# Kernel tuning notes

Measured on AMD Instinct MI355X. Metric: run time of the kernel, lower is better.

## Reference

```python
import jax, jax.numpy as jnp
import numpy as np

N = 50000
E = 1600000
HID = 128
K = 2
EPS = 0.3


def setup_inputs() -> dict:
    key = jax.random.key(0)
    ks = jax.random.split(key, 8)
    x = jax.random.normal(ks[0], (N, 512), dtype=jnp.float32)
    edge_index = jax.random.randint(ks[1], (2, E), 0, N, dtype=jnp.int32)
    t1_w = jax.random.normal(ks[2], (HID, 512), dtype=jnp.float32) * (1.414 / np.sqrt(512))
    t1_b = jnp.zeros((HID,), dtype=jnp.float32)
    gate_w = jax.random.normal(ks[3], (K, 2 * HID), dtype=jnp.float32) * (1.414 / np.sqrt(2 * HID))
    gate_b = jnp.zeros((K,), dtype=jnp.float32)
    t2_w = jax.random.normal(ks[4], (40, HID), dtype=jnp.float32) * (1.414 / np.sqrt(HID))
    t2_b = jnp.zeros((40,), dtype=jnp.float32)
    return {"x": x, "edge_index": edge_index, "t1_w": t1_w, "t1_b": t1_b,
            "gate_w": gate_w, "gate_b": gate_b, "t2_w": t2_w, "t2_b": t2_b}


def reference(x, edge_index, t1_w, t1_b, gate_w, gate_b, t2_w, t2_b):
    row, col = edge_index[0], edge_index[1]
    # degree(row, num_nodes=N).clamp(min=1) ** -0.5
    deg = jax.ops.segment_sum(jnp.ones((E,), dtype=x.dtype), row, num_segments=N)
    norm_degree = jnp.clip(deg, 1.0) ** -0.5  # [N]

    h = jax.nn.relu(x @ t1_w.T + t1_b)  # [N, HID]
    raw = h
    for k in range(K):
        # gate(cat([h[row], h[col]], 1)) == h[row] @ W[:H] + h[col] @ W[H:]
        w_r, w_c = gate_w[k, :HID], gate_w[k, HID:]
        g = jnp.tanh(h[row] @ w_r + h[col] @ w_c + gate_b[k])  # [E]
        norm = g * norm_degree[row] * norm_degree[col]          # [E]
        # message: norm * x_j (x_j = h[row], source), scatter-add at col (target)
        agg = jax.ops.segment_sum(norm[:, None] * h[row], col, num_segments=N)
        h = EPS * raw + agg
    logits = h @ t2_w.T + t2_b  # [N, 40]
    return jax.nn.log_softmax(logits, axis=1)
```

## Files before the change

### kernel.cpp

```cpp
#include <hip/hip_runtime.h>
#include <hip/hip_bf16.h>
#include <hip/hip_fp16.h>

#define N_NODES 50000
#define N_EDGES 1600000
#define HIDDEN  128
#define EPS_C   0.3f
#define NWORDS  12500
#define CHUNK   12500
#define NCHUNK  128

typedef _Float16 f16x8 __attribute__((ext_vector_type(8)));
typedef _Float16 f16x4 __attribute__((ext_vector_type(4)));
typedef float    f32x16 __attribute__((ext_vector_type(16)));

__global__ __launch_bounds__(256) void k_hist(const int* __restrict__ ei, unsigned int* __restrict__ part) {
    __shared__ unsigned int hist[NWORDS];
    int b = blockIdx.x;
    int type  = b >> 7;
    int chunk = b & 127;
    const int* src = ei + (size_t)type * N_EDGES + (size_t)chunk * CHUNK;
    for (int i = threadIdx.x; i < NWORDS; i += 256) hist[i] = 0;
    __syncthreads();
    for (int i = threadIdx.x; i < CHUNK; i += 256) {
        int v = src[i];
        atomicAdd(&hist[v >> 2], 1u << ((v & 3) * 8));
    }
    __syncthreads();
    unsigned int* dst = part + ((size_t)type * NCHUNK + chunk) * NWORDS;
    for (int i = threadIdx.x; i < NWORDS; i += 256) dst[i] = hist[i];
}

__global__ __launch_bounds__(256) void k_reduce(const unsigned int* __restrict__ part,
                                                float* __restrict__ nd, int* __restrict__ cnt,
                                                unsigned short* __restrict__ cntpre) {
    int w = blockIdx.x * 256 + threadIdx.x;
    if (w >= NWORDS) return;
    unsigned int s0 = 0, s1 = 0, s2 = 0, s3 = 0;
    const unsigned int* dp = part + w;
    for (int b = 0; b < NCHUNK; ++b) {
        unsigned int v = dp[(size_t)b * NWORDS];
        s0 += v & 255u; s1 += (v >> 8) & 255u; s2 += (v >> 16) & 255u; s3 += v >> 24;
    }
    nd[4 * w + 0] = rsqrtf(fmaxf((float)s0, 1.f));
    nd[4 * w + 1] = rsqrtf(fmaxf((float)s1, 1.f));
    nd[4 * w + 2] = rsqrtf(fmaxf((float)s2, 1.f));
    nd[4 * w + 3] = rsqrtf(fmaxf((float)s3, 1.f));
    const unsigned int* cp = part + (size_t)NCHUNK * NWORDS + w;
    unsigned int r0 = 0, r1 = 0, r2 = 0, r3 = 0;
    for (int b = 0; b < NCHUNK; ++b) {
        size_t o = (size_t)b * N_NODES + 4 * w;
        *(ushort4*)&cntpre[o] = make_ushort4((unsigned short)r0, (unsigned short)r1,
                                             (unsigned short)r2, (unsigned short)r3);
        unsigned int v = cp[(size_t)b * NWORDS];
        r0 += v & 255u; r1 += (v >> 8) & 255u; r2 += (v >> 16) & 255u; r3 += v >> 24;
    }
    cnt[4 * w + 0] = (int)r0;
    cnt[4 * w + 1] = (int)r1;
    cnt[4 * w + 2] = (int)r2;
    cnt[4 * w + 3] = (int)r3;
}

__global__ __launch_bounds__(256) void k_scan_a(const int* __restrict__ cnt,
                                                int* __restrict__ out, int* __restrict__ partials) {
    __shared__ int sh[256];
    int t = threadIdx.x;
    int base = blockIdx.x * 1024 + t * 4;
    int v0 = (base + 0 < N_NODES) ? cnt[base + 0] : 0;
    int v1 = (base + 1 < N_NODES) ? cnt[base + 1] : 0;
    int v2 = (base + 2 < N_NODES) ? cnt[base + 2] : 0;
    int v3 = (base + 3 < N_NODES) ? cnt[base + 3] : 0;
    int s = v0 + v1 + v2 + v3;
    sh[t] = s;
    __syncthreads();
    for (int off = 1; off < 256; off <<= 1) {
        int add = (t >= off) ? sh[t - off] : 0;
        __syncthreads();
        sh[t] += add;
        __syncthreads();
    }
    int excl = sh[t] - s;
    if (t == 255) partials[blockIdx.x] = sh[255];
    if (base + 0 < N_NODES) out[base + 0] = excl;
    if (base + 1 < N_NODES) out[base + 1] = excl + v0;
    if (base + 2 < N_NODES) out[base + 2] = excl + v0 + v1;
    if (base + 3 < N_NODES) out[base + 3] = excl + v0 + v1 + v2;
}

__global__ void k_scan_b(int* partials, int* colptr, int nb) {
    if (threadIdx.x == 0 && blockIdx.x == 0) {
        int run = 0;
        for (int i = 0; i < nb; ++i) { int t = partials[i]; partials[i] = run; run += t; }
        colptr[N_NODES] = run;
    }
}

__global__ void k_scan_c(int* __restrict__ colptr, const int* __restrict__ partials) {
    int i = blockIdx.x * blockDim.x + threadIdx.x;
    if (i >= N_NODES) return;
    colptr[i] += partials[i >> 10];
}

__global__ __launch_bounds__(256) void k_scatter2(const int* __restrict__ ei, const int* __restrict__ colptr,
                                                  const unsigned short* __restrict__ cntpre,
                                                  int* __restrict__ csr) {
    __shared__ unsigned int rank[NWORDS];
    int b = blockIdx.x;
    for (int i = threadIdx.x; i < NWORDS; i += 256) rank[i] = 0;
    __syncthreads();
    const int* rs = ei + (size_t)b * CHUNK;
    const int* cs = ei + N_EDGES + (size_t)b * CHUNK;
    const unsigned short* pre = cntpre + (size_t)b * N_NODES;
    for (int i = threadIdx.x; i < CHUNK; i += 256) {
        int r = rs[i];
        int c = cs[i];
        unsigned int old = atomicAdd(&rank[c >> 2], 1u << ((c & 3) * 8));
        unsigned int lr = (old >> ((c & 3) * 8)) & 255u;
        int pos = colptr[c] + (int)pre[c] + (int)lr;
        csr[pos] = r;
    }
}

__global__ void k_cvt(const float4* __restrict__ src, __half2* __restrict__ dst, int n4) {
    int i = blockIdx.x * 256 + threadIdx.x;
    if (i >= n4) return;
    float4 v = src[i];
    dst[2 * i]     = __floats2half2_rn(v.x, v.y);
    dst[2 * i + 1] = __floats2half2_rn(v.z, v.w);
}

__global__ __launch_bounds__(256) void k_gemm1(const float* __restrict__ x, const _Float16* __restrict__ wh,
                                               const float* __restrict__ bias, float* __restrict__ h,
                                               _Float16* __restrict__ hb) {
    __shared__ _Float16 As[64 * 64];
    __shared__ _Float16 Bs[128 * 64];
    int t = threadIdx.x;
    int wave = t >> 6;
    int lane = t & 63;
    int lm   = lane & 31;
    int half = lane >> 5;
    int mstrip = wave & 1;
    int nstrip = wave >> 1;

    int m0  = blockIdx.x * 64;
    int wm0 = m0 + mstrip * 32;
    int n0  = nstrip * 64;

    int aidx[4], arow[4], ac4[4];
    int bidx, brow[4], bg[4];
#pragma unroll
    for (int i = 0; i < 4; ++i) {
        aidx[i] = i * 256 + t;
        arow[i] = aidx[i] >> 4;
        ac4[i]  = aidx[i] & 15;
        bidx    = i * 256 + t;
        brow[i] = bidx >> 3;
        bg[i]   = bidx & 7;
    }

    float4 pa[4];
    f16x8  pb[4];
#define LOAD_TILES(K0)                                                                    \
    {                                                                                     \
        _Pragma("unroll")                                                                 \
        for (int i = 0; i < 4; ++i) {                                                     \
            int gr = m0 + arow[i]; if (gr >= N_NODES) gr = N_NODES - 1;                   \
            pa[i] = *(const float4*)(x + (size_t)gr * 512 + (K0) + ac4[i] * 4);           \
            pb[i] = *(const f16x8*)(wh + (size_t)brow[i] * 512 + (K0) + bg[i] * 8);       \
        }                                                                                 \
    }

    f32x16 acc0, acc1;
#pragma unroll
    for (int i = 0; i < 16; ++i) { acc0[i] = 0.f; acc1[i] = 0.f; }

    int ar = mstrip * 32 + lm;
    int brA = n0 + lm;
    int brB = n0 + 32 + lm;

    LOAD_TILES(0);
    for (int k0 = 0; k0 < 512; k0 += 64) {
#pragma unroll
        for (int i = 0; i < 4; ++i) {
            f16x4 a;
            a[0] = (_Float16)pa[i].x; a[1] = (_Float16)pa[i].y;
            a[2] = (_Float16)pa[i].z; a[3] = (_Float16)pa[i].w;
            int g = ac4[i] >> 1;
            *(f16x4*)&As[arow[i] * 64 + (((g ^ (arow[i] & 7)) << 3)) + (ac4[i] & 1) * 4] = a;
            *(f16x8*)&Bs[brow[i] * 64 + ((bg[i] ^ (brow[i] & 7)) << 3)] = pb[i];
        }
        __syncthreads();
        if (k0 + 64 < 512) LOAD_TILES(k0 + 64);
#pragma unroll
        for (int kk = 0; kk < 4; ++kk) {
            int ag = kk * 2 + half;
            f16x8 av  = *(const f16x8*)&As[ar  * 64 + ((ag ^ (ar  & 7)) << 3)];
            f16x8 bv0 = *(const f16x8*)&Bs[brA * 64 + ((ag ^ (brA & 7)) << 3)];
            f16x8 bv1 = *(const f16x8*)&Bs[brB * 64 + ((ag ^ (brA & 7)) << 3)];
            acc0 = __builtin_amdgcn_mfma_f32_32x32x16_f16(av, bv0, acc0, 0, 0, 0);
            acc1 = __builtin_amdgcn_mfma_f32_32x32x16_f16(av, bv1, acc1, 0, 0, 0);
        }
        __syncthreads();
    }
#undef LOAD_TILES

    float bs0 = bias[n0 + lm];
    float bs1 = bias[n0 + 32 + lm];
#pragma unroll
    for (int reg = 0; reg < 16; ++reg) {
        int row = (reg & 3) + 8 * (reg >> 2) + 4 * half;
        int gm = wm0 + row;
        if (gm < N_NODES) {
            float v0 = fmaxf(acc0[reg] + bs0, 0.f);
            float v1 = fmaxf(acc1[reg] + bs1, 0.f);
            h[(size_t)gm * HIDDEN + n0 + lm]      = v0;
            h[(size_t)gm * HIDDEN + n0 + 32 + lm] = v1;
            hb[(size_t)gm * HIDDEN + n0 + lm]      = (_Float16)v0;
            hb[(size_t)gm * HIDDEN + n0 + 32 + lm] = (_Float16)v1;
        }
    }
}

__global__ __launch_bounds__(256) void k_dot(const float* __restrict__ h, const float* __restrict__ gw,
                                             const float* __restrict__ gb, const float* __restrict__ nd,
                                             int layer, float2* __restrict__ dn, float* __restrict__ dcb) {
    int node = blockIdx.x * 4 + (threadIdx.x >> 6);
    int lane = threadIdx.x & 63;
    if (node >= N_NODES) return;
    const float2* hv = (const float2*)h;
    float2 wr = ((const float2*)(gw + layer * 256))[lane];
    float2 wc = ((const float2*)(gw + layer * 256 + 128))[lane];
    float2 hc = hv[(size_t)node * 64 + lane];
    float a = hc.x * wr.x + hc.y * wr.y;
    float b = hc.x * wc.x + hc.y * wc.y;
#pragma unroll
    for (int off = 32; off >= 1; off >>= 1) {
        a += __shfl_xor(a, off, 64);
        b += __shfl_xor(b, off, 64);
    }
    if (lane == 0) {
        dn[node]  = make_float2(a, nd[node]);
        dcb[node] = b + gb[layer];
    }
}

__global__ __launch_bounds__(256) void k_edgew(const int* __restrict__ csr, const int* __restrict__ colptr,
                                               const float2* __restrict__ dn, const float* __restrict__ dcb,
                                               float* __restrict__ warr) {
    int node = blockIdx.x * 8 + (threadIdx.x >> 5);
    int sl   = threadIdx.x & 31;
    if (node >= N_NODES) return;
    float dc  = dcb[node];
    int beg = colptr[node], end = colptr[node + 1];
    for (int p = beg + sl; p < end; p += 32) {
        int r = csr[p];
        float2 v = dn[r];
        float xx = v.x + dc;
        float t = __expf(2.0f * xx);
        float g = 1.0f - 2.0f / (t + 1.0f);
        warr[p] = g * v.y;
    }
}

__global__ __launch_bounds__(256) void k_prop(const __half2* __restrict__ hb, const float* __restrict__ raw,
                                              const int* __restrict__ colptr, const int* __restrict__ csr,
                                              const float* __restrict__ warr, const float* __restrict__ nd,
                                              float* __restrict__ hn, __half2* __restrict__ hbn) {
    int lane = threadIdx.x & 63;
    int node = __builtin_amdgcn_readfirstlane(blockIdx.x * 4 + (threadIdx.x >> 6));
    int beg = __builtin_amdgcn_readfirstlane(colptr[node]);
    int end = __builtin_amdgcn_readfirstlane(colptr[node + 1]);
    float acc0 = 0.f, acc1 = 0.f;
    int p = beg;
    for (; p + 8 <= end; p += 8) {
        int r0 = csr[p + 0], r1 = csr[p + 1], r2 = csr[p + 2], r3 = csr[p + 3];
        int r4 = csr[p + 4], r5 = csr[p + 5], r6 = csr[p + 6], r7 = csr[p + 7];
        float w0 = warr[p + 0], w1 = warr[p + 1], w2 = warr[p + 2], w3 = warr[p + 3];
        float w4 = warr[p + 4], w5 = warr[p + 5], w6 = warr[p + 6], w7 = warr[p + 7];
        __half2 v0 = hb[(size_t)r0 * 64 + lane];
        __half2 v1 = hb[(size_t)r1 * 64 + lane];
        __half2 v2 = hb[(size_t)r2 * 64 + lane];
        __half2 v3 = hb[(size_t)r3 * 64 + lane];
        __half2 v4 = hb[(size_t)r4 * 64 + lane];
        __half2 v5 = hb[(size_t)r5 * 64 + lane];
        __half2 v6 = hb[(size_t)r6 * 64 + lane];
        __half2 v7 = hb[(size_t)r7 * 64 + lane];
        acc0 = fmaf(w0, __low2float(v0), acc0);  acc1 = fmaf(w0, __high2float(v0), acc1);
        acc0 = fmaf(w1, __low2float(v1), acc0);  acc1 = fmaf(w1, __high2float(v1), acc1);
        acc0 = fmaf(w2, __low2float(v2), acc0);  acc1 = fmaf(w2, __high2float(v2), acc1);
        acc0 = fmaf(w3, __low2float(v3), acc0);  acc1 = fmaf(w3, __high2float(v3), acc1);
        acc0 = fmaf(w4, __low2float(v4), acc0);  acc1 = fmaf(w4, __high2float(v4), acc1);
        acc0 = fmaf(w5, __low2float(v5), acc0);  acc1 = fmaf(w5, __high2float(v5), acc1);
        acc0 = fmaf(w6, __low2float(v6), acc0);  acc1 = fmaf(w6, __high2float(v6), acc1);
        acc0 = fmaf(w7, __low2float(v7), acc0);  acc1 = fmaf(w7, __high2float(v7), acc1);
    }
    for (; p < end; ++p) {
        int r = csr[p];
        float w = warr[p];
        __half2 v = hb[(size_t)r * 64 + lane];
        acc0 = fmaf(w, __low2float(v), acc0);
        acc1 = fmaf(w, __high2float(v), acc1);
    }
    float ndc = nd[node];
    float2 rw = ((const float2*)raw)[(size_t)node * 64 + lane];
    float2 o;
    o.x = fmaf(EPS_C, rw.x, ndc * acc0);
    o.y = fmaf(EPS_C, rw.y, ndc * acc1);
    if (hn)  ((float2*)hn)[(size_t)node * 64 + lane] = o;
    if (hbn) hbn[(size_t)node * 64 + lane] = __floats2half2_rn(o.x, o.y);
}

__global__ __launch_bounds__(256) void k_out(const float* __restrict__ h, const float* __restrict__ w2,
                                             const float* __restrict__ b2, float* __restrict__ out) {
    __shared__ float w2t[128][40];
    __shared__ float hs[4][128];
    int wid  = threadIdx.x >> 6;
    int lane = threadIdx.x & 63;
    int node = blockIdx.x * 4 + wid;

    for (int idx = threadIdx.x; idx < 40 * 128; idx += 256) {
        int j = idx >> 7;
        int i = idx & 127;
        w2t[i][j] = w2[idx];
    }
    if (node < N_NODES) {
        const float2* hvv = (const float2*)h;
        float2 v = hvv[(size_t)node * 64 + lane];
        hs[wid][2 * lane]     = v.x;
        hs[wid][2 * lane + 1] = v.y;
    }
    __syncthreads();
    if (node < N_NODES) {
        int j = lane;
        float logit = -INFINITY;
        if (j < 40) {
            float a = 0.f;
#pragma unroll 8
            for (int i = 0; i < 128; ++i) a = fmaf(hs[wid][i], w2t[i][j], a);
            logit = a + b2[j];
        }
        float mx = logit;
#pragma unroll
        for (int off = 32; off >= 1; off >>= 1) mx = fmaxf(mx, __shfl_xor(mx, off, 64));
        float ex = (j < 40) ? expf(logit - mx) : 0.f;
        float sum = ex;
#pragma unroll
        for (int off = 32; off >= 1; off >>= 1) sum += __shfl_xor(sum, off, 64);
        float ls = logf(sum);
        if (j < 40) out[(size_t)node * 40 + j] = logit - mx - ls;
    }
}

extern "C" void kernel_launch(void* const* d_in, const int* in_sizes, int n_in,
                              void* d_out, int out_size, void* d_ws, size_t ws_size,
                              hipStream_t stream) {
    const float* x   = (const float*)d_in[0];
    const int*   ei  = (const int*)  d_in[1];
    const float* t1w = (const float*)d_in[2];
    const float* t1b = (const float*)d_in[3];
    const float* gw  = (const float*)d_in[4];
    const float* gb  = (const float*)d_in[5];
    const float* w2  = (const float*)d_in[6];
    const float* b2  = (const float*)d_in[7];
    float* out = (float*)d_out;

    char* p = (char*)d_ws;
    int*    colptr   = (int*)p;    p += (size_t)(N_NODES + 64) * 4;
    int*    partials = (int*)p;    p += 256 * 4;
    float*  nd       = (float*)p;  p += (size_t)N_NODES * 4;
    int*    cnt      = (int*)p;    p += (size_t)N_NODES * 4;
    float*  dcb      = (float*)p;  p += (size_t)N_NODES * 4;
    float2* dn       = (float2*)p; p += (size_t)N_NODES * 8;
    int*    csr      = (int*)p;    p += (size_t)N_EDGES * 4;
    float*  warr     = (float*)p;  p += (size_t)N_EDGES * 4;
    _Float16* wh     = (_Float16*)p; p += (size_t)HIDDEN * 512 * 2;
    char* q = p;
    unsigned int*   part   = (unsigned int*)q;
    unsigned short* cntpre = (unsigned short*)(q + (size_t)2 * NCHUNK * NWORDS * 4);
    __half2* hb0 = (__half2*)p; p += (size_t)N_NODES * 64 * 4;
    __half2* hb1 = (__half2*)p; p += (size_t)N_NODES * 64 * 4;
    float*  h0   = (float*)p;   p += (size_t)N_NODES * HIDDEN * 4;
    float*  h1   = (float*)p;   p += (size_t)N_NODES * HIDDEN * 4;
    float*  h2   = (float*)p;   p += (size_t)N_NODES * HIDDEN * 4;

    k_hist<<<2 * NCHUNK, 256, 0, stream>>>(ei, part);
    k_reduce<<<(NWORDS + 255) / 256, 256, 0, stream>>>(part, nd, cnt, cntpre);
    int nb = (N_NODES + 1023) / 1024;
    k_scan_a<<<nb, 256, 0, stream>>>(cnt, colptr, partials);
    k_scan_b<<<1, 64, 0, stream>>>(partials, colptr, nb);
    k_scan_c<<<(N_NODES + 255) / 256, 256, 0, stream>>>(colptr, partials);
    k_scatter2<<<NCHUNK, 256, 0, stream>>>(ei, colptr, cntpre, csr);

    k_cvt<<<(16384 + 255) / 256, 256, 0, stream>>>((const float4*)t1w, (__half2*)wh, 16384);
    k_gemm1<<<(N_NODES + 63) / 64, 256, 0, stream>>>(x, wh, t1b, h0, (_Float16*)hb0);

    k_dot  <<<(N_NODES + 3) / 4, 256, 0, stream>>>(h0, gw, gb, nd, 0, dn, dcb);
    k_edgew<<<(N_NODES + 7) / 8, 256, 0, stream>>>(csr, colptr, dn, dcb, warr);
    k_prop <<<(N_NODES + 3) / 4, 256, 0, stream>>>(hb0, h0, colptr, csr, warr, nd, h1, hb1);

    k_dot  <<<(N_NODES + 3) / 4, 256, 0, stream>>>(h1, gw, gb, nd, 1, dn, dcb);
    k_edgew<<<(N_NODES + 7) / 8, 256, 0, stream>>>(csr, colptr, dn, dcb, warr);
    k_prop <<<(N_NODES + 3) / 4, 256, 0, stream>>>(hb1, h0, colptr, csr, warr, nd, h2, (__half2*)nullptr);

    k_out<<<(N_NODES + 3) / 4, 256, 0, stream>>>(h2, w2, b2, out);
}
```

Before: 518.6 us.

## Compute output projection with fp16 MFMA and write final hidden as fp16

The final propagation now writes only an fp16 copy of the hidden state instead of fp32. The output layer reads that fp16 state and computes the 40-wide projection with 32x32x16 MFMA instructions against a zero-padded fp16 copy of the weights. The fused log-softmax is then done with 32-lane shuffles. This replaces the scalar LDS-based dot product and halves the hidden-state traffic, at the cost of fp16 rounding in the final layer and one extra small conversion launch.

```diff
diff --git a/kernel.cpp b/kernel.cpp
--- a/kernel.cpp
+++ b/kernel.cpp
@@ -127,6 +127,20 @@
     float4 v = src[i];
     dst[2 * i]     = __floats2half2_rn(v.x, v.y);
     dst[2 * i + 1] = __floats2half2_rn(v.z, v.w);
+}
+
+__global__ void k_cvtw(const float4* __restrict__ src, __half2* __restrict__ dst, int n4src, int n4tot) {
+    int i = blockIdx.x * 256 + threadIdx.x;
+    if (i >= n4tot) return;
+    if (i < n4src) {
+        float4 v = src[i];
+        dst[2 * i]     = __floats2half2_rn(v.x, v.y);
+        dst[2 * i + 1] = __floats2half2_rn(v.z, v.w);
+    } else {
+        __half2 z = __floats2half2_rn(0.f, 0.f);
+        dst[2 * i]     = z;
+        dst[2 * i + 1] = z;
+    }
 }
 
 __global__ __launch_bounds__(256) void k_gemm1(const float* __restrict__ x, const _Float16* __restrict__ wh,
@@ -310,44 +324,54 @@
     if (hbn) hbn[(size_t)node * 64 + lane] = __floats2half2_rn(o.x, o.y);
 }
 
-__global__ __launch_bounds__(256) void k_out(const float* __restrict__ h, const float* __restrict__ w2,
+__global__ __launch_bounds__(256) void k_out(const _Float16* __restrict__ h16, const _Float16* __restrict__ w2h,
                                              const float* __restrict__ b2, float* __restrict__ out) {
-    __shared__ float w2t[128][40];
-    __shared__ float hs[4][128];
-    int wid  = threadIdx.x >> 6;
+    int wave = threadIdx.x >> 6;
     int lane = threadIdx.x & 63;
-    int node = blockIdx.x * 4 + wid;
-
-    for (int idx = threadIdx.x; idx < 40 * 128; idx += 256) {
-        int j = idx >> 7;
-        int i = idx & 127;
-        w2t[i][j] = w2[idx];
-    }
-    if (node < N_NODES) {
-        const float2* hvv = (const float2*)h;
-        float2 v = hvv[(size_t)node * 64 + lane];
-        hs[wid][2 * lane]     = v.x;
-        hs[wid][2 * lane + 1] = v.y;
-    }
-    __syncthreads();
-    if (node < N_NODES) {
-        int j = lane;
-        float logit = -INFINITY;
-        if (j < 40) {
-            float a = 0.f;
-#pragma unroll 8
-            for (int i = 0; i < 128; ++i) a = fmaf(hs[wid][i], w2t[i][j], a);
-            logit = a + b2[j];
+    int lm   = lane & 31;
+    int half = lane >> 5;
+
+    int wm0 = blockIdx.x * 128 + wave * 32;
+    int m   = wm0 + lm;
+    int mc  = (m < N_NODES) ? m : (N_NODES - 1);
+
+    const _Float16* arow  = h16 + (size_t)mc * HIDDEN + half * 8;
+    const _Float16* brow0 = w2h + (size_t)lm * HIDDEN + half * 8;
+    const _Float16* brow1 = w2h + (size_t)(32 + lm) * HIDDEN + half * 8;
+
+    f32x16 acc0, acc1;
+#pragma unroll
+    for (int i = 0; i < 16; ++i) { acc0[i] = 0.f; acc1[i] = 0.f; }
+
+#pragma unroll
+    for (int k0 = 0; k0 < 128; k0 += 16) {
+        f16x8 av = *(const f16x8*)(arow  + k0);
+        f16x8 b0 = *(const f16x8*)(brow0 + k0);
+        f16x8 b1 = *(const f16x8*)(brow1 + k0);
+        acc0 = __builtin_amdgcn_mfma_f32_32x32x16_f16(av, b0, acc0, 0, 0, 0);
+        acc1 = __builtin_amdgcn_mfma_f32_32x32x16_f16(av, b1, acc1, 0, 0, 0);
+    }
+
+    float bj0 = b2[lm];
+    float bj1 = (lm < 8) ? b2[32 + lm] : 0.f;
+
+#pragma unroll
+    for (int reg = 0; reg < 16; ++reg) {
+        int row = (reg & 3) + 8 * (reg >> 2) + 4 * half;
+        float v0 = acc0[reg] + bj0;
+        float v1 = (lm < 8) ? (acc1[reg] + bj1) : -INFINITY;
+        float mx = fmaxf(v0, v1);
+#pragma unroll
+        for (int off = 16; off >= 1; off >>= 1) mx = fmaxf(mx, __shfl_xor(mx, off, 64));
+        float s = __expf(v0 - mx) + ((lm < 8) ? __expf(v1 - mx) : 0.f);
+#pragma unroll
+        for (int off = 16; off >= 1; off >>= 1) s += __shfl_xor(s, off, 64);
+        float ls = __logf(s) + mx;
+        int gm = wm0 + row;
+        if (gm < N_NODES) {
+            out[(size_t)gm * 40 + lm] = v0 - ls;
+            if (lm < 8) out[(size_t)gm * 40 + 32 + lm] = v1 - ls;
         }
-        float mx = logit;
-#pragma unroll
-        for (int off = 32; off >= 1; off >>= 1) mx = fmaxf(mx, __shfl_xor(mx, off, 64));
-        float ex = (j < 40) ? expf(logit - mx) : 0.f;
-        float sum = ex;
-#pragma unroll
-        for (int off = 32; off >= 1; off >>= 1) sum += __shfl_xor(sum, off, 64);
-        float ls = logf(sum);
-        if (j < 40) out[(size_t)node * 40 + j] = logit - mx - ls;
     }
 }
 
@@ -374,14 +398,15 @@
     int*    csr      = (int*)p;    p += (size_t)N_EDGES * 4;
     float*  warr     = (float*)p;  p += (size_t)N_EDGES * 4;
     _Float16* wh     = (_Float16*)p; p += (size_t)HIDDEN * 512 * 2;
+    _Float16* w2h    = (_Float16*)p; p += (size_t)64 * HIDDEN * 2;
     char* q = p;
     unsigned int*   part   = (unsigned int*)q;
     unsigned short* cntpre = (unsigned short*)(q + (size_t)2 * NCHUNK * NWORDS * 4);
     __half2* hb0 = (__half2*)p; p += (size_t)N_NODES * 64 * 4;
     __half2* hb1 = (__half2*)p; p += (size_t)N_NODES * 64 * 4;
+    __half2* hb2 = (__half2*)p; p += (size_t)N_NODES * 64 * 4;
     float*  h0   = (float*)p;   p += (size_t)N_NODES * HIDDEN * 4;
     float*  h1   = (float*)p;   p += (size_t)N_NODES * HIDDEN * 4;
-    float*  h2   = (float*)p;   p += (size_t)N_NODES * HIDDEN * 4;
 
     k_hist<<<2 * NCHUNK, 256, 0, stream>>>(ei, part);
     k_reduce<<<(NWORDS + 255) / 256, 256, 0, stream>>>(part, nd, cnt, cntpre);
@@ -392,6 +417,7 @@
     k_scatter2<<<NCHUNK, 256, 0, stream>>>(ei, colptr, cntpre, csr);
 
     k_cvt<<<(16384 + 255) / 256, 256, 0, stream>>>((const float4*)t1w, (__half2*)wh, 16384);
+    k_cvtw<<<8, 256, 0, stream>>>((const float4*)w2, (__half2*)w2h, 40 * HIDDEN / 4, 64 * HIDDEN / 4);
     k_gemm1<<<(N_NODES + 63) / 64, 256, 0, stream>>>(x, wh, t1b, h0, (_Float16*)hb0);
 
     k_dot  <<<(N_NODES + 3) / 4, 256, 0, stream>>>(h0, gw, gb, nd, 0, dn, dcb);
@@ -400,7 +426,7 @@
 
     k_dot  <<<(N_NODES + 3) / 4, 256, 0, stream>>>(h1, gw, gb, nd, 1, dn, dcb);
     k_edgew<<<(N_NODES + 7) / 8, 256, 0, stream>>>(csr, colptr, dn, dcb, warr);
-    k_prop <<<(N_NODES + 3) / 4, 256, 0, stream>>>(hb1, h0, colptr, csr, warr, nd, h2, (__half2*)nullptr);
-
-    k_out<<<(N_NODES + 3) / 4, 256, 0, stream>>>(h2, w2, b2, out);
-}
+    k_prop <<<(N_NODES + 3) / 4, 256, 0, stream>>>(hb1, h0, colptr, csr, warr, nd, (float*)nullptr, hb2);
+
+    k_out<<<(N_NODES + 127) / 128, 256, 0, stream>>>((const _Float16*)hb2, w2h, b2, out);
+}
```

Result: faster. 470.2 us (-9.3%).
